# Performance work log

Measured on AMD Instinct MI355X. Metric: run time of the kernel, lower is better.

The kernel has to match this reference:

```python
import jax, jax.numpy as jnp
from jax import lax
import numpy as np

# larq-style ste_sign: forward sign (with sign(0)=+1), straight-through grad clipped to |x|<=1
@jax.custom_vjp
def ste_sign(x):
    return jnp.where(x >= 0, 1.0, -1.0).astype(x.dtype)

def _ste_fwd(x):
    return ste_sign(x), x

def _ste_bwd(x, g):
    return (g * (jnp.abs(x) <= 1.0).astype(g.dtype),)

ste_sign.defvjp(_ste_fwd, _ste_bwd)


def setup_inputs() -> dict:
    key = jax.random.key(0)
    k1, k2 = jax.random.split(key)
    B, H, Wd, Cin = 16, 256, 256, 32
    M, kh, kw, Cout = 4, 3, 3, 32
    x = jax.random.normal(k1, (B, H, Wd, Cin), dtype=jnp.float32)
    W = jax.random.normal(k2, (M, kh, kw, Cin, Cout), dtype=jnp.float32)
    b = jnp.zeros((M, Cout), dtype=jnp.float32)
    return {"x": x, "W": W, "b": b}


def reference(x, W, b):
    # Multibin: sum_{m} QuantConv2D_m(x).  Each branch binarizes the SAME input,
    # so sum of convs == one conv with the sum of the binarized kernels (fused).
    xq = ste_sign(x)                 # [B,H,W,Cin], values in {-1,+1}
    wq = ste_sign(W)                 # [M,kh,kw,Cin,Cout]
    w_sum = wq.sum(axis=0)           # [kh,kw,Cin,Cout]
    y = lax.conv_general_dilated(
        xq, w_sum,
        window_strides=(1, 1),
        padding="SAME",
        dimension_numbers=("NHWC", "HWIO", "NHWC"),
    )
    return y + b.sum(axis=0)         # [B,H,W,Cout]
```

## Files before the change

kernel.cpp:

```cpp
#include <hip/hip_runtime.h>


#define RH     8
#define NSTAGE 34
#define PITCH  40
#define SLOT   (NSTAGE * PITCH)

typedef __attribute__((ext_vector_type(8)))  __bf16 bf16x8;
typedef __attribute__((ext_vector_type(16))) float  f32x16;

__device__ __forceinline__ unsigned int pack2(float a, float b, bool ok) {
    unsigned int lo = ok ? ((a >= 0.0f) ? 0x3F80u : 0xBF80u) : 0u;
    unsigned int hi = ok ? ((b >= 0.0f) ? 0x3F80u : 0xBF80u) : 0u;
    return lo | (hi << 16);
}

__global__ void prep_kernel(const float* __restrict__ W, const float* __restrict__ bias,
                            unsigned short* __restrict__ wsT, float* __restrict__ bsum) {
    int t = blockIdx.x * 256 + threadIdx.x;
    if (t < 9216) {
        int k   = t >> 5;
        int co  = t & 31;
        int tap = k >> 5;
        int ci  = k & 31;
        float s = 0.0f;
        #pragma unroll
        for (int m = 0; m < 4; ++m) {
            float w = W[(m * 9 + tap) * 1024 + ci * 32 + co];
            s += (w >= 0.0f) ? 1.0f : -1.0f;
        }
        unsigned int u = __builtin_bit_cast(unsigned int, s);
        wsT[co * 288 + k] = (unsigned short)(u >> 16);
    }
    if (t < 32) {
        float s = 0.0f;
        #pragma unroll
        for (int m = 0; m < 4; ++m) s += bias[m * 32 + t];
        bsum[t] = s;
    }
}

__device__ __forceinline__ void stage_row(const float* __restrict__ x,
                                          unsigned short* __restrict__ dst,
                                          int bimg, int c0, int absrow, int lane) {
    bool rowok = (absrow >= 0) && (absrow < 256);
    const float* rowp = x + (long)((bimg * 256 + absrow) * 256) * 32;
    #pragma unroll
    for (int p = 0; p < 5; ++p) {
        int f = lane + p * 64;
        int pix = f >> 3, ch = f & 7;
        if (pix < NSTAGE) {
            int col = c0 - 1 + pix;
            bool ok = rowok && (col >= 0) && (col < 256);
            float4 v = ok ? *(const float4*)(rowp + col * 32 + ch * 4)
                          : make_float4(0.f, 0.f, 0.f, 0.f);
            *(uint2*)(dst + pix * PITCH + ch * 4) =
                make_uint2(pack2(v.x, v.y, ok), pack2(v.z, v.w, ok));
        }
    }
}

__global__ __launch_bounds__(64) void conv_kernel(const float* __restrict__ x,
                                                  const unsigned short* __restrict__ wsT,
                                                  const float* __restrict__ bsum,
                                                  float* __restrict__ out) {
    __shared__ unsigned short lds[4 * SLOT];

    const int lane = threadIdx.x;
    const int lrow = lane & 31;
    const int lk   = lane >> 5;

    const int bs   = blockIdx.x;
    const int c0   = (bs & 7) * 32;
    const int r0   = ((bs >> 3) & 31) * RH;
    const int bimg = bs >> 8;

    bf16x8 bfrag[18];
    #pragma unroll
    for (int t = 0; t < 18; ++t)
        bfrag[t] = *(const bf16x8*)(wsT + lrow * 288 + t * 16 + lk * 8);
    const float bsv = bsum[lrow];

    #pragma unroll
    for (int pre = 0; pre < 3; ++pre)
        stage_row(x, lds + pre * SLOT, bimg, c0, r0 - 1 + pre, lane);

    const int a_base = lrow * PITCH + lk * 8;

    for (int i = 0; i < RH; ++i) {
        const int r = r0 + i;
        const bool do_pf = (i < RH - 1);
        const int absrow = r + 2;
        const bool rowok = do_pf && (absrow < 256);
        const float* rowp = x + (long)((bimg * 256 + absrow) * 256) * 32;

        float4 buf[5];
        #pragma unroll
        for (int p = 0; p < 5; ++p) {
            int f = lane + p * 64;
            int pix = f >> 3, ch = f & 7;
            int col = c0 - 1 + pix;
            bool ok = rowok && (pix < NSTAGE) && (col >= 0) && (col < 256);
            buf[p] = ok ? *(const float4*)(rowp + col * 32 + ch * 4)
                        : make_float4(0.f, 0.f, 0.f, 0.f);
        }

        f32x16 acc = {};
        #pragma unroll
        for (int dh = 0; dh < 3; ++dh) {
            const unsigned short* sb = lds + ((i + dh) & 3) * SLOT + a_base;
            #pragma unroll
            for (int dw = 0; dw < 3; ++dw) {
                #pragma unroll
                for (int hf = 0; hf < 2; ++hf) {
                    bf16x8 a = *(const bf16x8*)(sb + dw * PITCH + hf * 16);
                    acc = __builtin_amdgcn_mfma_f32_32x32x16_bf16(
                              a, bfrag[(dh * 3 + dw) * 2 + hf], acc, 0, 0, 0);
                }
            }
        }

        float* op = out + ((long)((bimg * 256 + r) * 256 + c0)) * 32 + lrow;
        #pragma unroll
        for (int reg = 0; reg < 16; ++reg) {
            int pr = (reg & 3) + 8 * (reg >> 2) + 4 * lk;
            op[pr * 32] = acc[reg] + bsv;
        }

        if (do_pf) {
            unsigned short* dst = lds + ((i + 3) & 3) * SLOT;
            #pragma unroll
            for (int p = 0; p < 5; ++p) {
                int f = lane + p * 64;
                int pix = f >> 3, ch = f & 7;
                if (pix < NSTAGE) {
                    int col = c0 - 1 + pix;
                    bool ok = (absrow < 256) && (col >= 0) && (col < 256);
                    *(uint2*)(dst + pix * PITCH + ch * 4) =
                        make_uint2(pack2(buf[p].x, buf[p].y, ok),
                                   pack2(buf[p].z, buf[p].w, ok));
                }
            }
        }
    }
}

extern "C" void kernel_launch(void* const* d_in, const int* in_sizes, int n_in,
                              void* d_out, int out_size, void* d_ws, size_t ws_size,
                              hipStream_t stream) {
    const float* x    = (const float*)d_in[0];
    const float* W    = (const float*)d_in[1];
    const float* bias = (const float*)d_in[2];
    float* out = (float*)d_out;

    unsigned short* wsT = (unsigned short*)d_ws;
    float* bsum = (float*)((char*)d_ws + 18432);

    prep_kernel<<<36, 256, 0, stream>>>(W, bias, wsT, bsum);
    conv_kernel<<<4096, 64, 0, stream>>>(x, wsT, bsum, out);
}
```

Measured before the change: 272.7 us.

## Move binarized weights from registers to shared LDS and use two-wave blocks

Each block now runs two waves that cover adjacent 32-column tiles. The per-lane weight fragments are no longer held in 18 vector registers; they are written to LDS once and read back before every MFMA. The goal is to cut VGPR pressure and share the weight staging between waves. In exchange, every MFMA now needs an extra LDS read. LDS per block also grows to about 40KB, which may cap the number of waves per CU more tightly than the register savings allow.

```diff
diff --git a/kernel.cpp b/kernel.cpp
--- a/kernel.cpp
+++ b/kernel.cpp
@@ -5,6 +5,7 @@
 #define NSTAGE 34
 #define PITCH  40
 #define SLOT   (NSTAGE * PITCH)
+#define BLDS   9216
 
 typedef __attribute__((ext_vector_type(8)))  __bf16 bf16x8;
 typedef __attribute__((ext_vector_type(16))) float  f32x16;
@@ -60,32 +61,38 @@
     }
 }
 
-__global__ __launch_bounds__(64) void conv_kernel(const float* __restrict__ x,
-                                                  const unsigned short* __restrict__ wsT,
-                                                  const float* __restrict__ bsum,
-                                                  float* __restrict__ out) {
-    __shared__ unsigned short lds[4 * SLOT];
+__global__ __launch_bounds__(128) void conv_kernel(const float* __restrict__ x,
+                                                   const unsigned short* __restrict__ wsT,
+                                                   const float* __restrict__ bsum,
+                                                   float* __restrict__ out) {
+    __shared__ unsigned short lds[BLDS + 2 * 4 * SLOT];
 
-    const int lane = threadIdx.x;
+    const int tid  = threadIdx.x;
+    const int lane = tid & 63;
+    const int wv   = tid >> 6;
     const int lrow = lane & 31;
     const int lk   = lane >> 5;
 
     const int bs   = blockIdx.x;
-    const int c0   = (bs & 7) * 32;
-    const int r0   = ((bs >> 3) & 31) * RH;
-    const int bimg = bs >> 8;
+    const int c0   = (bs & 3) * 64 + wv * 32;
+    const int r0   = ((bs >> 2) & 31) * RH;
+    const int bimg = bs >> 7;
 
-    bf16x8 bfrag[18];
     #pragma unroll
-    for (int t = 0; t < 18; ++t)
-        bfrag[t] = *(const bf16x8*)(wsT + lrow * 288 + t * 16 + lk * 8);
+    for (int t = 0; t < 18; ++t) {
+        uint4 v = *(const uint4*)(wsT + lrow * 288 + t * 16 + lk * 8);
+        *(uint4*)(lds + (t * 64 + lane) * 8) = v;
+    }
     const float bsv = bsum[lrow];
+
+    unsigned short* slots = lds + BLDS + wv * (4 * SLOT);
 
     #pragma unroll
     for (int pre = 0; pre < 3; ++pre)
-        stage_row(x, lds + pre * SLOT, bimg, c0, r0 - 1 + pre, lane);
+        stage_row(x, slots + pre * SLOT, bimg, c0, r0 - 1 + pre, lane);
 
     const int a_base = lrow * PITCH + lk * 8;
+    const unsigned short* bbase = lds + lane * 8;
 
     for (int i = 0; i < RH; ++i) {
         const int r = r0 + i;
@@ -108,14 +115,15 @@
         f32x16 acc = {};
         #pragma unroll
         for (int dh = 0; dh < 3; ++dh) {
-            const unsigned short* sb = lds + ((i + dh) & 3) * SLOT + a_base;
+            const unsigned short* sa = slots + ((i + dh) & 3) * SLOT + a_base;
             #pragma unroll
             for (int dw = 0; dw < 3; ++dw) {
                 #pragma unroll
                 for (int hf = 0; hf < 2; ++hf) {
-                    bf16x8 a = *(const bf16x8*)(sb + dw * PITCH + hf * 16);
-                    acc = __builtin_amdgcn_mfma_f32_32x32x16_bf16(
-                              a, bfrag[(dh * 3 + dw) * 2 + hf], acc, 0, 0, 0);
+                    int tap = (dh * 3 + dw) * 2 + hf;
+                    bf16x8 a = *(const bf16x8*)(sa + dw * PITCH + hf * 16);
+                    bf16x8 b = *(const bf16x8*)(bbase + tap * 512);
+                    acc = __builtin_amdgcn_mfma_f32_32x32x16_bf16(a, b, acc, 0, 0, 0);
                 }
             }
         }
@@ -128,7 +136,7 @@
         }
 
         if (do_pf) {
-            unsigned short* dst = lds + ((i + 3) & 3) * SLOT;
+            unsigned short* dst = slots + ((i + 3) & 3) * SLOT;
             #pragma unroll
             for (int p = 0; p < 5; ++p) {
                 int f = lane + p * 64;
@@ -157,5 +165,5 @@
     float* bsum = (float*)((char*)d_ws + 18432);
 
     prep_kernel<<<36, 256, 0, stream>>>(W, bias, wsT, bsum);
-    conv_kernel<<<4096, 64, 0, stream>>>(x, wsT, bsum, out);
+    conv_kernel<<<2048, 128, 0, stream>>>(x, wsT, bsum, out);
 }
```

New measurement: 289.0 us. 1.06x slower.
